# Optimization experiments

Hardware: AMD Instinct MI355X
Metric: run time of the kernel (lower is better)

Reference implementation:

```python
import jax, jax.numpy as jnp
import numpy as np

K = 1024
H = 16
HEAD = K // H

def setup_inputs() -> dict:
    key = jax.random.key(0)
    ks = jax.random.split(key, 6)
    b, t = 2, 2048
    x = jax.random.normal(ks[0], (b, t, K), dtype=jnp.float32)
    padding = jnp.ones((b, t), dtype=jnp.int32)
    s = 1.0 / np.sqrt(K)
    Wq = jax.random.normal(ks[1], (K, K), dtype=jnp.float32) * s
    Wk = jax.random.normal(ks[2], (K, K), dtype=jnp.float32) * s
    Wv = jax.random.normal(ks[3], (K, K), dtype=jnp.float32) * s
    Wo = jax.random.normal(ks[4], (K, K), dtype=jnp.float32) * s
    bo = jnp.zeros((K,), dtype=jnp.float32)
    return {"x": x, "padding": padding, "Wq": Wq, "Wk": Wk, "Wv": Wv, "Wo": Wo, "bo": bo}

def reference(x, padding, Wq, Wk, Wv, Wo, bo):
    b, t, k = x.shape
    h, d = H, HEAD
    # projections (nn.Linear: x @ W.T), then split heads -> [b,h,t,d]
    q = (x @ Wq.T).reshape(b, t, h, d).transpose(0, 2, 1, 3)
    kk = (x @ Wk.T).reshape(b, t, h, d).transpose(0, 2, 1, 3)
    v = (x @ Wv.T).reshape(b, t, h, d).transpose(0, 2, 1, 3)
    scores = jnp.einsum('bhqd,bhkd->bhqk', q, kk)
    # key-side padding mask: positions with padding==0 get -inf (before scaling,
    # same result since -inf/sqrt(d) == -inf)
    mask = (padding == 0)[:, None, None, :]  # [b,1,1,t]
    scores = jnp.where(mask, -jnp.inf, scores) / np.sqrt(d).astype(np.float32)
    weights = jax.nn.softmax(scores, axis=-1)
    out = jnp.einsum('bhqk,bhkd->bhqd', weights, v)
    out = out.transpose(0, 2, 1, 3).reshape(b, t, h * d)
    return out @ Wo.T + bo
```

## Files before the change

kernel.cpp:

```cpp
#include <hip/hip_runtime.h>
#include <hip/hip_bf16.h>
#include <cmath>
#include <stdint.h>

#define K_DIM 1024
#define NH    16
#define HD    64
#define T     2048
#define NTOK  4096
#define NBH   32

typedef __bf16 bf16x8 __attribute__((ext_vector_type(8)));
typedef float  f32x4  __attribute__((ext_vector_type(4)));

__device__ __forceinline__ unsigned short f2bf(float f) {
  union { float f; unsigned u; } v; v.f = f;
  unsigned u = v.u;
  return (unsigned short)((u + 0x7FFFu + ((u >> 16) & 1u)) >> 16);
}
__device__ __forceinline__ ushort4 pk4(float a, float b, float c, float d) {
  union { __hip_bfloat162 h[2]; ushort4 u; } r;
  r.h[0] = __float22bfloat162_rn(float2{a, b});
  r.h[1] = __float22bfloat162_rn(float2{c, d});
  return r.u;
}

__device__ __forceinline__ void gload16(const void* g, void* l) {
  __builtin_amdgcn_global_load_lds(
      (__attribute__((address_space(1))) void*)(g),
      (__attribute__((address_space(3))) void*)(l),
      16, 0, 0);
}

__global__ void convert_kernel(const float* __restrict__ x,
                               const float* __restrict__ Wq,
                               const float* __restrict__ Wk,
                               const float* __restrict__ Wv,
                               const float* __restrict__ Wo,
                               unsigned short* __restrict__ xb,
                               unsigned short* __restrict__ wqkv,
                               unsigned short* __restrict__ wob)
{
  const size_t NX = (size_t)NTOK * K_DIM;
  const size_t NW = (size_t)K_DIM * K_DIM;
  size_t i = ((size_t)blockIdx.x * blockDim.x + threadIdx.x) * 4;
  const float* src; unsigned short* dst; size_t off;
  float scale = 1.f;
  if (i < NX)             { src = x;  dst = xb;          off = i; }
  else if (i < NX + NW)   { src = Wq; dst = wqkv;        off = i - NX;
                            scale = 0.18033688011112042f; }
  else if (i < NX + 2*NW) { src = Wk; dst = wqkv + NW;   off = i - NX - NW; }
  else if (i < NX + 3*NW) { src = Wv; dst = wqkv + 2*NW; off = i - NX - 2*NW; }
  else                    { src = Wo; dst = wob;         off = i - NX - 3*NW; }
  float4 v = *(const float4*)(src + off);
  *(ushort4*)(dst + off) = pk4(v.x * scale, v.y * scale, v.z * scale, v.w * scale);
}

template <int MODE, int TM, int TN>
__global__ __launch_bounds__(256, 2)
void gemm_bt(const unsigned short* __restrict__ A,
             const unsigned short* __restrict__ B,
             unsigned short* __restrict__ o_q,
             unsigned short* __restrict__ o_k,
             unsigned short* __restrict__ o_v,
             float* __restrict__ o_f,
             const float* __restrict__ bias)
{
  __shared__ unsigned short Asm[TM * 64];
  __shared__ unsigned short Bsm[TN * 64];
  const int tid  = threadIdx.x;
  const int wave = tid >> 6;
  const int lane = tid & 63;
  const int lq   = lane & 15;
  const int quad = lane >> 4;
  const int bm = blockIdx.x, bn = blockIdx.y;
  const int wm = (wave >> 1) * (TM / 2), wn = (wave & 1) * (TN / 2);
  const int MT = TM / 32, NT = TN / 32;

  f32x4 acc[MT][NT];
#pragma unroll
  for (int i = 0; i < MT; ++i)
#pragma unroll
    for (int j = 0; j < NT; ++j) acc[i][j] = (f32x4){0.f, 0.f, 0.f, 0.f};

  const char* Ab = (const char*)(A + (size_t)bm * TM * K_DIM);
  const char* Bb = (const char*)(B + (size_t)bn * TN * K_DIM);

  for (int k0 = 0; k0 < K_DIM; k0 += 64) {
#pragma unroll
    for (int i = 0; i < MT; ++i) {
      int off   = i * 4096 + wave * 1024 + lane * 16;
      int row   = off >> 7;
      int chunk = (off >> 4) & 7;
      int scol  = (chunk ^ (row & 7)) << 4;
      gload16(Ab + (size_t)row * (K_DIM * 2) + (size_t)k0 * 2 + scol,
              (char*)Asm + off - lane * 16);
    }
#pragma unroll
    for (int i = 0; i < NT; ++i) {
      int off   = i * 4096 + wave * 1024 + lane * 16;
      int row   = off >> 7;
      int chunk = (off >> 4) & 7;
      int scol  = (chunk ^ (row & 7)) << 4;
      gload16(Bb + (size_t)row * (K_DIM * 2) + (size_t)k0 * 2 + scol,
              (char*)Bsm + off - lane * 16);
    }
    __syncthreads();
#pragma unroll
    for (int kk = 0; kk < 64; kk += 32) {
      bf16x8 af[MT], bfr[NT];
#pragma unroll
      for (int mt = 0; mt < MT; ++mt) {
        int row = wm + mt * 16 + lq;
        int sw  = (quad + (kk >> 3)) ^ (row & 7);
        af[mt] = *(const bf16x8*)((const char*)Asm + row * 128 + (sw << 4));
      }
#pragma unroll
      for (int nt = 0; nt < NT; ++nt) {
        int row = wn + nt * 16 + lq;
        int sw  = (quad + (kk >> 3)) ^ (row & 7);
        bfr[nt] = *(const bf16x8*)((const char*)Bsm + row * 128 + (sw << 4));
      }
#pragma unroll
      for (int mt = 0; mt < MT; ++mt)
#pragma unroll
        for (int nt = 0; nt < NT; ++nt)
          acc[mt][nt] = __builtin_amdgcn_mfma_f32_16x16x32_bf16(af[mt], bfr[nt], acc[mt][nt], 0, 0, 0);
    }
    __syncthreads();
  }

#pragma unroll
  for (int mt = 0; mt < MT; ++mt) {
    int mbase = bm * TM + wm + mt * 16 + quad * 4;
#pragma unroll
    for (int nt = 0; nt < NT; ++nt) {
      int n = bn * TN + wn + nt * 16 + lq;
      if (MODE == 1) {
        int which = mbase >> 10, c = mbase & 1023;
        int h = c >> 6, d0 = c & 63;
        int b = n >> 11, t = n & 2047;
        if (which < 2) {
          ushort4 pk = pk4(acc[mt][nt][0], acc[mt][nt][1], acc[mt][nt][2], acc[mt][nt][3]);
          unsigned short* dst = which ? o_k : o_q;
          *(ushort4*)&dst[((size_t)(b * NH + h) * T + t) * HD + d0] = pk;
        } else {
#pragma unroll
          for (int r = 0; r < 4; ++r)
            o_v[((size_t)(b * NH + h) * HD + d0 + r) * T + t] = f2bf(acc[mt][nt][r]);
        }
      } else {
        float4 bv = *(const float4*)&bias[mbase];
        float4 o;
        o.x = acc[mt][nt][0] + bv.x; o.y = acc[mt][nt][1] + bv.y;
        o.z = acc[mt][nt][2] + bv.z; o.w = acc[mt][nt][3] + bv.w;
        *(float4*)&o_f[(size_t)n * K_DIM + mbase] = o;
      }
    }
  }
}

__global__ __launch_bounds__(256, 2)
void attn_kernel(const unsigned short* __restrict__ Q,
                 const unsigned short* __restrict__ Kb,
                 const unsigned short* __restrict__ Vt,
                 const int* __restrict__ padding,
                 unsigned short* __restrict__ O)
{
  __shared__ unsigned short Ksm[128 * 64];
  __shared__ unsigned short Vsm[2][64 * 128];
  __shared__ unsigned short Plds[4][32 * 32 * 4];

  const int tid  = threadIdx.x;
  const int wave = tid >> 6;
  const int lane = tid & 63;
  const int lq   = lane & 15;
  const int quad = lane >> 4;
  const int bh = blockIdx.x;
  const int qt = blockIdx.y;
  const int b  = bh >> 4;
  const int h  = bh & 15;
  const int qbase = qt * 128 + wave * 32;

  bf16x8 qf[2][2];
#pragma unroll
  for (int nq = 0; nq < 2; ++nq)
#pragma unroll
    for (int kk = 0; kk < 2; ++kk)
      qf[nq][kk] = *(const bf16x8*)&Q[((size_t)bh * T + qbase + nq * 16 + lq) * HD + kk * 32 + quad * 8];

  f32x4 o_acc[4][2];
#pragma unroll
  for (int md = 0; md < 4; ++md)
#pragma unroll
    for (int nq = 0; nq < 2; ++nq) o_acc[md][nq] = (f32x4){0.f, 0.f, 0.f, 0.f};
  float l_part[2] = {0.f, 0.f};

  auto stage = [&](int kt, int buf) {
#pragma unroll
    for (int i = 0; i < 4; ++i) {
      int off = i * 4096 + wave * 1024 + lane * 16;
      {
        int row = off >> 7, chunk = (off >> 4) & 7;
        int scol = (chunk ^ (row & 7)) << 4;
        gload16((const char*)Kb + ((size_t)(bh * T + kt * 128 + row) * HD) * 2 + scol,
                (char*)Ksm + off - lane * 16);
      }
      {
        int row = off >> 8, chunk = (off >> 4) & 15;
        int scol = (chunk ^ (row & 15)) << 4;
        gload16((const char*)Vt + ((size_t)(bh * HD + row) * T + (size_t)kt * 128) * 2 + scol,
                (char*)Vsm[buf] + off - lane * 16);
      }
    }
  };

  stage(0, 0);
  __syncthreads();

  for (int kt = 0; kt < T / 128; ++kt) {
    const int cur = kt & 1;

    f32x4 st[8][2];
#pragma unroll
    for (int nt = 0; nt < 8; ++nt)
#pragma unroll
      for (int nq = 0; nq < 2; ++nq) st[nt][nq] = (f32x4){0.f, 0.f, 0.f, 0.f};
#pragma unroll
    for (int kk = 0; kk < 2; ++kk) {
#pragma unroll
      for (int nt = 0; nt < 8; ++nt) {
        int row = nt * 16 + lq;
        int sw  = (quad + kk * 4) ^ (row & 7);
        bf16x8 kf = *(const bf16x8*)((const char*)Ksm + row * 128 + (sw << 4));
        st[nt][0] = __builtin_amdgcn_mfma_f32_16x16x32_bf16(kf, qf[0][kk], st[nt][0], 0, 0, 0);
        st[nt][1] = __builtin_amdgcn_mfma_f32_16x16x32_bf16(kf, qf[1][kk], st[nt][1], 0, 0, 0);
      }
    }

    __syncthreads();

    if (kt < T / 128 - 1) stage(kt + 1, cur ^ 1);

#pragma unroll
    for (int nt = 0; nt < 8; ++nt) {
      int4 pd = *(const int4*)&padding[b * T + kt * 128 + nt * 16 + quad * 4];
#pragma unroll
      for (int nq = 0; nq < 2; ++nq) {
        float p0 = pd.x ? __builtin_amdgcn_exp2f(st[nt][nq][0]) : 0.f;
        float p1 = pd.y ? __builtin_amdgcn_exp2f(st[nt][nq][1]) : 0.f;
        float p2 = pd.z ? __builtin_amdgcn_exp2f(st[nt][nq][2]) : 0.f;
        float p3 = pd.w ? __builtin_amdgcn_exp2f(st[nt][nq][3]) : 0.f;
        l_part[nq] += (p0 + p1) + (p2 + p3);
        int row = nt * 4 + quad;
        int col = nq * 16 + lq;
        *(ushort4*)&Plds[wave][(row * 32 + col) * 4] = pk4(p0, p1, p2, p3);
      }
    }
    asm volatile("s_waitcnt lgkmcnt(0)" ::: "memory");

#pragma unroll
    for (int kk = 0; kk < 4; ++kk) {
      bf16x8 pf[2];
#pragma unroll
      for (int nq = 0; nq < 2; ++nq) {
        int row0 = kk * 8 + quad * 2;
        ushort4 lo = *(const ushort4*)&Plds[wave][((row0    ) * 32 + nq * 16 + lq) * 4];
        ushort4 hi = *(const ushort4*)&Plds[wave][((row0 + 1) * 32 + nq * 16 + lq) * 4];
        union { ushort4 u[2]; bf16x8 v; } cvt;
        cvt.u[0] = lo; cvt.u[1] = hi;
        pf[nq] = cvt.v;
      }
#pragma unroll
      for (int md = 0; md < 4; ++md) {
        int row = md * 16 + lq;
        int sw  = ((kk * 4 + quad) ^ (row & 15)) << 4;
        bf16x8 vf = *(const bf16x8*)((const char*)Vsm[cur] + row * 256 + sw);
        o_acc[md][0] = __builtin_amdgcn_mfma_f32_16x16x32_bf16(vf, pf[0], o_acc[md][0], 0, 0, 0);
        o_acc[md][1] = __builtin_amdgcn_mfma_f32_16x16x32_bf16(vf, pf[1], o_acc[md][1], 0, 0, 0);
      }
    }

    __syncthreads();
  }

  float inv[2];
#pragma unroll
  for (int nq = 0; nq < 2; ++nq) {
    float lsum = l_part[nq];
    lsum += __shfl_xor(lsum, 16);
    lsum += __shfl_xor(lsum, 32);
    inv[nq] = (lsum > 0.f) ? 1.f / lsum : 0.f;
  }
#pragma unroll
  for (int md = 0; md < 4; ++md) {
#pragma unroll
    for (int nq = 0; nq < 2; ++nq) {
      int t = qbase + nq * 16 + lq;
      int chan0 = h * HD + md * 16 + quad * 4;
      *(ushort4*)&O[((size_t)(b * T + t)) * K_DIM + chan0] =
          pk4(o_acc[md][nq][0] * inv[nq], o_acc[md][nq][1] * inv[nq],
              o_acc[md][nq][2] * inv[nq], o_acc[md][nq][3] * inv[nq]);
    }
  }
}

extern "C" void kernel_launch(void* const* d_in, const int* in_sizes, int n_in,
                              void* d_out, int out_size, void* d_ws, size_t ws_size,
                              hipStream_t stream)
{
  const float* x       = (const float*)d_in[0];
  const int*   padding = (const int*)d_in[1];
  const float* Wq      = (const float*)d_in[2];
  const float* Wk      = (const float*)d_in[3];
  const float* Wv      = (const float*)d_in[4];
  const float* Wo      = (const float*)d_in[5];
  const float* bo      = (const float*)d_in[6];
  float* out = (float*)d_out;

  char* ws = (char*)d_ws;
  unsigned short* xb   = (unsigned short*)(ws);
  unsigned short* wqkv = (unsigned short*)(ws + (8u  << 20));
  unsigned short* wob  = (unsigned short*)(ws + (14u << 20));
  unsigned short* qb   = (unsigned short*)(ws + (16u << 20));
  unsigned short* kb   = (unsigned short*)(ws + (24u << 20));
  unsigned short* vtb  = (unsigned short*)(ws + (32u << 20));
  unsigned short* ab   = (unsigned short*)(ws + (40u << 20));

  convert_kernel<<<8192, 256, 0, stream>>>(x, Wq, Wk, Wv, Wo, xb, wqkv, wob);

  gemm_bt<1, 192, 128><<<dim3(16, 32), 256, 0, stream>>>(wqkv, xb, qb, kb, vtb, nullptr, nullptr);

  attn_kernel<<<dim3(32, 16), 256, 0, stream>>>(qb, kb, vtb, padding, ab);

  gemm_bt<2, 64, 128><<<dim3(16, 32), 256, 0, stream>>>(wob, ab, nullptr, nullptr, nullptr, out, bo);
}
```

Baseline: 185.0 us.

## Use 8 waves of 16 queries and pass P via shuffles instead of LDS

The attention kernel now runs 512 threads per block, with each wave owning 16 query rows instead of 32, which halves per-wave accumulators and allows higher occupancy. The per-wave P staging buffer in shared memory is removed. Probabilities are packed into bf16 pairs and redistributed across lanes with shuffles to form the PV MFMA operand. This removes LDS write/read traffic and a wait, but adds shuffle instructions and more waves reloading the same K/V fragments from LDS.

New measurement: 199.6 us. +7.9%, slower.

```diff
diff --git a/kernel.cpp b/kernel.cpp
--- a/kernel.cpp
+++ b/kernel.cpp
@@ -22,6 +22,11 @@
   union { __hip_bfloat162 h[2]; ushort4 u; } r;
   r.h[0] = __float22bfloat162_rn(float2{a, b});
   r.h[1] = __float22bfloat162_rn(float2{c, d});
+  return r.u;
+}
+__device__ __forceinline__ int pk2(float a, float b) {
+  union { __hip_bfloat162 h; int u; } r;
+  r.h = __float22bfloat162_rn(float2{a, b});
   return r.u;
 }
 
@@ -160,7 +165,7 @@
   }
 }
 
-__global__ __launch_bounds__(256, 2)
+__global__ __launch_bounds__(512, 4)
 void attn_kernel(const unsigned short* __restrict__ Q,
                  const unsigned short* __restrict__ Kb,
                  const unsigned short* __restrict__ Vt,
@@ -169,7 +174,6 @@
 {
   __shared__ unsigned short Ksm[128 * 64];
   __shared__ unsigned short Vsm[2][64 * 128];
-  __shared__ unsigned short Plds[4][32 * 32 * 4];
 
   const int tid  = threadIdx.x;
   const int wave = tid >> 6;
@@ -180,26 +184,26 @@
   const int qt = blockIdx.y;
   const int b  = bh >> 4;
   const int h  = bh & 15;
-  const int qbase = qt * 128 + wave * 32;
-
-  bf16x8 qf[2][2];
-#pragma unroll
-  for (int nq = 0; nq < 2; ++nq)
-#pragma unroll
-    for (int kk = 0; kk < 2; ++kk)
-      qf[nq][kk] = *(const bf16x8*)&Q[((size_t)bh * T + qbase + nq * 16 + lq) * HD + kk * 32 + quad * 8];
-
-  f32x4 o_acc[4][2];
-#pragma unroll
-  for (int md = 0; md < 4; ++md)
-#pragma unroll
-    for (int nq = 0; nq < 2; ++nq) o_acc[md][nq] = (f32x4){0.f, 0.f, 0.f, 0.f};
-  float l_part[2] = {0.f, 0.f};
+  const int qbase = qt * 128 + wave * 16;
+
+  const int  xlo   = ((quad & 1) << 5) + lq;
+  const int  xhi   = xlo + 16;
+  const bool hiFam = quad >= 2;
+
+  bf16x8 qf[2];
+#pragma unroll
+  for (int kk = 0; kk < 2; ++kk)
+    qf[kk] = *(const bf16x8*)&Q[((size_t)bh * T + qbase + lq) * HD + kk * 32 + quad * 8];
+
+  f32x4 o_acc[4];
+#pragma unroll
+  for (int md = 0; md < 4; ++md) o_acc[md] = (f32x4){0.f, 0.f, 0.f, 0.f};
+  float l_part = 0.f;
 
   auto stage = [&](int kt, int buf) {
 #pragma unroll
-    for (int i = 0; i < 4; ++i) {
-      int off = i * 4096 + wave * 1024 + lane * 16;
+    for (int i = 0; i < 2; ++i) {
+      int off = i * 8192 + wave * 1024 + lane * 16;
       {
         int row = off >> 7, chunk = (off >> 4) & 7;
         int scol = (chunk ^ (row & 7)) << 4;
@@ -221,11 +225,9 @@
   for (int kt = 0; kt < T / 128; ++kt) {
     const int cur = kt & 1;
 
-    f32x4 st[8][2];
-#pragma unroll
-    for (int nt = 0; nt < 8; ++nt)
-#pragma unroll
-      for (int nq = 0; nq < 2; ++nq) st[nt][nq] = (f32x4){0.f, 0.f, 0.f, 0.f};
+    f32x4 st[8];
+#pragma unroll
+    for (int nt = 0; nt < 8; ++nt) st[nt] = (f32x4){0.f, 0.f, 0.f, 0.f};
 #pragma unroll
     for (int kk = 0; kk < 2; ++kk) {
 #pragma unroll
@@ -233,8 +235,7 @@
         int row = nt * 16 + lq;
         int sw  = (quad + kk * 4) ^ (row & 7);
         bf16x8 kf = *(const bf16x8*)((const char*)Ksm + row * 128 + (sw << 4));
-        st[nt][0] = __builtin_amdgcn_mfma_f32_16x16x32_bf16(kf, qf[0][kk], st[nt][0], 0, 0, 0);
-        st[nt][1] = __builtin_amdgcn_mfma_f32_16x16x32_bf16(kf, qf[1][kk], st[nt][1], 0, 0, 0);
+        st[nt] = __builtin_amdgcn_mfma_f32_16x16x32_bf16(kf, qf[kk], st[nt], 0, 0, 0);
       }
     }
 
@@ -242,65 +243,56 @@
 
     if (kt < T / 128 - 1) stage(kt + 1, cur ^ 1);
 
+    int bx[8][2];
 #pragma unroll
     for (int nt = 0; nt < 8; ++nt) {
       int4 pd = *(const int4*)&padding[b * T + kt * 128 + nt * 16 + quad * 4];
-#pragma unroll
-      for (int nq = 0; nq < 2; ++nq) {
-        float p0 = pd.x ? __builtin_amdgcn_exp2f(st[nt][nq][0]) : 0.f;
-        float p1 = pd.y ? __builtin_amdgcn_exp2f(st[nt][nq][1]) : 0.f;
-        float p2 = pd.z ? __builtin_amdgcn_exp2f(st[nt][nq][2]) : 0.f;
-        float p3 = pd.w ? __builtin_amdgcn_exp2f(st[nt][nq][3]) : 0.f;
-        l_part[nq] += (p0 + p1) + (p2 + p3);
-        int row = nt * 4 + quad;
-        int col = nq * 16 + lq;
-        *(ushort4*)&Plds[wave][(row * 32 + col) * 4] = pk4(p0, p1, p2, p3);
-      }
-    }
-    asm volatile("s_waitcnt lgkmcnt(0)" ::: "memory");
+      float p0 = pd.x ? __builtin_amdgcn_exp2f(st[nt][0]) : 0.f;
+      float p1 = pd.y ? __builtin_amdgcn_exp2f(st[nt][1]) : 0.f;
+      float p2 = pd.z ? __builtin_amdgcn_exp2f(st[nt][2]) : 0.f;
+      float p3 = pd.w ? __builtin_amdgcn_exp2f(st[nt][3]) : 0.f;
+      l_part += (p0 + p1) + (p2 + p3);
+      bx[nt][0] = pk2(p0, p1);
+      bx[nt][1] = pk2(p2, p3);
+    }
 
 #pragma unroll
     for (int kk = 0; kk < 4; ++kk) {
-      bf16x8 pf[2];
-#pragma unroll
-      for (int nq = 0; nq < 2; ++nq) {
-        int row0 = kk * 8 + quad * 2;
-        ushort4 lo = *(const ushort4*)&Plds[wave][((row0    ) * 32 + nq * 16 + lq) * 4];
-        ushort4 hi = *(const ushort4*)&Plds[wave][((row0 + 1) * 32 + nq * 16 + lq) * 4];
-        union { ushort4 u[2]; bf16x8 v; } cvt;
-        cvt.u[0] = lo; cvt.u[1] = hi;
-        pf[nq] = cvt.v;
-      }
+      int X0 = bx[2 * kk][0],     X1 = bx[2 * kk][1];
+      int Y0 = bx[2 * kk + 1][0], Y1 = bx[2 * kk + 1][1];
+      int ax0 = __shfl(X0, xlo), ay0 = __shfl(Y0, xlo);
+      int ax1 = __shfl(X1, xlo), ay1 = __shfl(Y1, xlo);
+      int bx0 = __shfl(X0, xhi), by0 = __shfl(Y0, xhi);
+      int bx1 = __shfl(X1, xhi), by1 = __shfl(Y1, xhi);
+      union { int d[4]; bf16x8 v; } pf;
+      pf.d[0] = hiFam ? ay0 : ax0;
+      pf.d[1] = hiFam ? ay1 : ax1;
+      pf.d[2] = hiFam ? by0 : bx0;
+      pf.d[3] = hiFam ? by1 : bx1;
 #pragma unroll
       for (int md = 0; md < 4; ++md) {
         int row = md * 16 + lq;
         int sw  = ((kk * 4 + quad) ^ (row & 15)) << 4;
         bf16x8 vf = *(const bf16x8*)((const char*)Vsm[cur] + row * 256 + sw);
-        o_acc[md][0] = __builtin_amdgcn_mfma_f32_16x16x32_bf16(vf, pf[0], o_acc[md][0], 0, 0, 0);
-        o_acc[md][1] = __builtin_amdgcn_mfma_f32_16x16x32_bf16(vf, pf[1], o_acc[md][1], 0, 0, 0);
+        o_acc[md] = __builtin_amdgcn_mfma_f32_16x16x32_bf16(vf, pf.v, o_acc[md], 0, 0, 0);
       }
     }
 
     __syncthreads();
   }
 
-  float inv[2];
-#pragma unroll
-  for (int nq = 0; nq < 2; ++nq) {
-    float lsum = l_part[nq];
-    lsum += __shfl_xor(lsum, 16);
-    lsum += __shfl_xor(lsum, 32);
-    inv[nq] = (lsum > 0.f) ? 1.f / lsum : 0.f;
-  }
-#pragma unroll
-  for (int md = 0; md < 4; ++md) {
-#pragma unroll
-    for (int nq = 0; nq < 2; ++nq) {
-      int t = qbase + nq * 16 + lq;
+  float lsum = l_part;
+  lsum += __shfl_xor(lsum, 16);
+  lsum += __shfl_xor(lsum, 32);
+  float inv = (lsum > 0.f) ? 1.f / lsum : 0.f;
+  {
+    int t = qbase + lq;
+#pragma unroll
+    for (int md = 0; md < 4; ++md) {
       int chan0 = h * HD + md * 16 + quad * 4;
       *(ushort4*)&O[((size_t)(b * T + t)) * K_DIM + chan0] =
-          pk4(o_acc[md][nq][0] * inv[nq], o_acc[md][nq][1] * inv[nq],
-              o_acc[md][nq][2] * inv[nq], o_acc[md][nq][3] * inv[nq]);
+          pk4(o_acc[md][0] * inv, o_acc[md][1] * inv,
+              o_acc[md][2] * inv, o_acc[md][3] * inv);
     }
   }
 }
@@ -331,7 +323,7 @@
 
   gemm_bt<1, 192, 128><<<dim3(16, 32), 256, 0, stream>>>(wqkv, xb, qb, kb, vtb, nullptr, nullptr);
 
-  attn_kernel<<<dim3(32, 16), 256, 0, stream>>>(qb, kb, vtb, padding, ab);
+  attn_kernel<<<dim3(32, 16), 512, 0, stream>>>(qb, kb, vtb, padding, ab);
 
   gemm_bt<2, 64, 128><<<dim3(16, 32), 256, 0, stream>>>(wob, ab, nullptr, nullptr, nullptr, out, bo);
 }
```

## Feed softmax probabilities to PV MFMA directly from registers, dropping LDS round-trip

Applied to the files above, without the earlier changes.

The exponentiated score tile already has the register layout the A operand of a 16x16x16 bf16 MFMA needs, so the P values stay in registers instead of being written to and read back from a per-wave LDS buffer. The PV product switches from 16x16x32 to 16x16x16bf16_1k instructions with the output accumulator transposed (query rows by head dim). This removes the LDS stores, the waitcnt and the P reloads, and frees the P shared buffer. The cost is twice as many smaller MFMAs, narrower V reads from LDS, and an epilogue that writes individual bf16 scalars with a shuffle per row instead of packed 4-wide stores.

Measured after the change: 188.7 us. +2.0%, slower.

```diff
diff --git a/kernel.cpp b/kernel.cpp
--- a/kernel.cpp
+++ b/kernel.cpp
@@ -12,6 +12,7 @@
 
 typedef __bf16 bf16x8 __attribute__((ext_vector_type(8)));
 typedef float  f32x4  __attribute__((ext_vector_type(4)));
+typedef short  s16x4  __attribute__((ext_vector_type(4)));
 
 __device__ __forceinline__ unsigned short f2bf(float f) {
   union { float f; unsigned u; } v; v.f = f;
@@ -22,6 +23,11 @@
   union { __hip_bfloat162 h[2]; ushort4 u; } r;
   r.h[0] = __float22bfloat162_rn(float2{a, b});
   r.h[1] = __float22bfloat162_rn(float2{c, d});
+  return r.u;
+}
+__device__ __forceinline__ int pk2(float a, float b) {
+  union { __hip_bfloat162 h; int u; } r;
+  r.h = __float22bfloat162_rn(float2{a, b});
   return r.u;
 }
 
@@ -169,7 +175,6 @@
 {
   __shared__ unsigned short Ksm[128 * 64];
   __shared__ unsigned short Vsm[2][64 * 128];
-  __shared__ unsigned short Plds[4][32 * 32 * 4];
 
   const int tid  = threadIdx.x;
   const int wave = tid >> 6;
@@ -189,11 +194,11 @@
     for (int kk = 0; kk < 2; ++kk)
       qf[nq][kk] = *(const bf16x8*)&Q[((size_t)bh * T + qbase + nq * 16 + lq) * HD + kk * 32 + quad * 8];
 
-  f32x4 o_acc[4][2];
-#pragma unroll
-  for (int md = 0; md < 4; ++md)
-#pragma unroll
-    for (int nq = 0; nq < 2; ++nq) o_acc[md][nq] = (f32x4){0.f, 0.f, 0.f, 0.f};
+  f32x4 o_acc[2][4];
+#pragma unroll
+  for (int nq = 0; nq < 2; ++nq)
+#pragma unroll
+    for (int nd = 0; nd < 4; ++nd) o_acc[nq][nd] = (f32x4){0.f, 0.f, 0.f, 0.f};
   float l_part[2] = {0.f, 0.f};
 
   auto stage = [&](int kt, int buf) {
@@ -242,6 +247,7 @@
 
     if (kt < T / 128 - 1) stage(kt + 1, cur ^ 1);
 
+    union PA { int d[2]; s16x4 v; } pa[8][2];
 #pragma unroll
     for (int nt = 0; nt < 8; ++nt) {
       int4 pd = *(const int4*)&padding[b * T + kt * 128 + nt * 16 + quad * 4];
@@ -252,55 +258,46 @@
         float p2 = pd.z ? __builtin_amdgcn_exp2f(st[nt][nq][2]) : 0.f;
         float p3 = pd.w ? __builtin_amdgcn_exp2f(st[nt][nq][3]) : 0.f;
         l_part[nq] += (p0 + p1) + (p2 + p3);
-        int row = nt * 4 + quad;
-        int col = nq * 16 + lq;
-        *(ushort4*)&Plds[wave][(row * 32 + col) * 4] = pk4(p0, p1, p2, p3);
-      }
-    }
-    asm volatile("s_waitcnt lgkmcnt(0)" ::: "memory");
-
-#pragma unroll
-    for (int kk = 0; kk < 4; ++kk) {
-      bf16x8 pf[2];
-#pragma unroll
-      for (int nq = 0; nq < 2; ++nq) {
-        int row0 = kk * 8 + quad * 2;
-        ushort4 lo = *(const ushort4*)&Plds[wave][((row0    ) * 32 + nq * 16 + lq) * 4];
-        ushort4 hi = *(const ushort4*)&Plds[wave][((row0 + 1) * 32 + nq * 16 + lq) * 4];
-        union { ushort4 u[2]; bf16x8 v; } cvt;
-        cvt.u[0] = lo; cvt.u[1] = hi;
-        pf[nq] = cvt.v;
-      }
-#pragma unroll
-      for (int md = 0; md < 4; ++md) {
-        int row = md * 16 + lq;
-        int sw  = ((kk * 4 + quad) ^ (row & 15)) << 4;
-        bf16x8 vf = *(const bf16x8*)((const char*)Vsm[cur] + row * 256 + sw);
-        o_acc[md][0] = __builtin_amdgcn_mfma_f32_16x16x32_bf16(vf, pf[0], o_acc[md][0], 0, 0, 0);
-        o_acc[md][1] = __builtin_amdgcn_mfma_f32_16x16x32_bf16(vf, pf[1], o_acc[md][1], 0, 0, 0);
+        pa[nt][nq].d[0] = pk2(p0, p1);
+        pa[nt][nq].d[1] = pk2(p2, p3);
+      }
+    }
+
+#pragma unroll
+    for (int nt = 0; nt < 8; ++nt) {
+#pragma unroll
+      for (int nd = 0; nd < 4; ++nd) {
+        int row = nd * 16 + lq;
+        int g   = 2 * nt + (quad >> 1);
+        int sw  = g ^ (row & 15);
+        s16x4 vf = *(const s16x4*)((const char*)Vsm[cur] + row * 256 + (sw << 4) + ((quad & 1) << 3));
+        o_acc[0][nd] = __builtin_amdgcn_mfma_f32_16x16x16bf16_1k(pa[nt][0].v, vf, o_acc[0][nd], 0, 0, 0);
+        o_acc[1][nd] = __builtin_amdgcn_mfma_f32_16x16x16bf16_1k(pa[nt][1].v, vf, o_acc[1][nd], 0, 0, 0);
       }
     }
 
     __syncthreads();
   }
 
-  float inv[2];
+  float linv[2];
 #pragma unroll
   for (int nq = 0; nq < 2; ++nq) {
     float lsum = l_part[nq];
     lsum += __shfl_xor(lsum, 16);
     lsum += __shfl_xor(lsum, 32);
-    inv[nq] = (lsum > 0.f) ? 1.f / lsum : 0.f;
-  }
-#pragma unroll
-  for (int md = 0; md < 4; ++md) {
-#pragma unroll
-    for (int nq = 0; nq < 2; ++nq) {
-      int t = qbase + nq * 16 + lq;
-      int chan0 = h * HD + md * 16 + quad * 4;
-      *(ushort4*)&O[((size_t)(b * T + t)) * K_DIM + chan0] =
-          pk4(o_acc[md][nq][0] * inv[nq], o_acc[md][nq][1] * inv[nq],
-              o_acc[md][nq][2] * inv[nq], o_acc[md][nq][3] * inv[nq]);
+    linv[nq] = (lsum > 0.f) ? 1.f / lsum : 0.f;
+  }
+#pragma unroll
+  for (int nq = 0; nq < 2; ++nq) {
+#pragma unroll
+    for (int r = 0; r < 4; ++r) {
+      float iv = __shfl(linv[nq], quad * 4 + r);
+      int t = qbase + nq * 16 + quad * 4 + r;
+#pragma unroll
+      for (int nd = 0; nd < 4; ++nd) {
+        int chan = h * HD + nd * 16 + lq;
+        O[((size_t)(b * T + t)) * K_DIM + chan] = f2bf(o_acc[nq][nd][r] * iv);
+      }
     }
   }
 }
```
